# Performance work log

Measured on AMD Instinct MI355X. Metric: run time of the kernel, lower is better.

## Reference

```python
import jax, jax.numpy as jnp
import numpy as np

BATCH = 2048
DIMS = [256, 256, 256, 128]  # input, hidden, hidden, output
N_ATOMS = 4  # identity, sin, tanh, square


def setup_inputs() -> dict:
    key = jax.random.key(0)
    ks = jax.random.split(key, 8)
    inp = {"x": jax.random.normal(ks[0], (BATCH, DIMS[0]), dtype=jnp.float32)}
    for li in range(3):
        out_d, in_d = DIMS[li + 1], DIMS[li]
        inp[f"W{li}"] = jax.random.normal(ks[1 + li], (out_d, in_d), dtype=jnp.float32) * 0.1
        inp[f"b{li}"] = jnp.zeros((out_d,), dtype=jnp.float32)
        inp[f"f_idx{li}"] = jax.random.randint(ks[4 + li], (out_d, in_d), 0, N_ATOMS, dtype=jnp.int32)
    return inp


def _w_eff(W, idx):
    # per-element atom nonlinearity selected by idx: [identity, sin, tanh, square]
    atoms = jnp.stack([W, jnp.sin(W), jnp.tanh(W), W * W], axis=0)  # [A, out, in]
    return jnp.take_along_axis(atoms, idx[None].astype(jnp.int32), axis=0)[0]


def reference(x, W0, b0, W1, b1, W2, b2, f_idx0, f_idx1, f_idx2):
    layers = [(W0, b0, f_idx0), (W1, b1, f_idx1), (W2, b2, f_idx2)]
    h = x
    n = len(layers)
    for li, (W, b, idx) in enumerate(layers):
        We = _w_eff(W, idx)                       # [out, in]
        z = h[:, None, :] * We[None, :, :]        # [batch, out, in]
        gz = z if li == n - 1 else jnp.tanh(z)    # g_fixed='tanh' on hidden layers
        h = gz.sum(axis=-1) + b[None, :]          # [batch, out]
    return h
```

## Files before the change

### kernel.cpp

```cpp
#include <hip/hip_runtime.h>
#include <math.h>


__device__ __forceinline__ float fast_rcp(float x)  { return __builtin_amdgcn_rcpf(x); }
__device__ __forceinline__ float fast_exp2(float x) { return __builtin_amdgcn_exp2f(x); }

#define SC  2.885390081777927f
#define INV (1.0f / 2.885390081777927f)
#define INV2PI 0.15915494309189535f

__global__ void weff_kernel(const float* __restrict__ W0, const int* __restrict__ I0,
                            const float* __restrict__ W1, const int* __restrict__ I1,
                            const float* __restrict__ W2, const int* __restrict__ I2,
                            float* __restrict__ ws) {
    int tid = blockIdx.x * blockDim.x + threadIdx.x;
    const float* W; const int* I; float* out; int outd; int e;
    if (tid < 65536)        { W = W0; I = I0; out = ws;          outd = 256; e = tid; }
    else if (tid < 131072)  { W = W1; I = I1; out = ws + 65536;  outd = 256; e = tid - 65536; }
    else if (tid < 163840)  { W = W2; I = I2; out = ws + 131072; outd = 128; e = tid - 131072; }
    else return;
    int o = e >> 8;
    int i = e & 255;
    float w = W[e];
    int idx = I[e];
    float sn = __builtin_amdgcn_sinf(w * INV2PI);
    float th = 1.0f - 2.0f * fast_rcp(fast_exp2(w * SC) + 1.0f);
    float sq = w * w;
    float v = (idx == 1) ? sn : (idx == 2) ? th : (idx == 3) ? sq : w;
    out[(i >> 2) * (outd * 4) + o * 4 + (i & 3)] = v;
}

__global__ __launch_bounds__(1024, 8) void mlp_kernel(
    const float* __restrict__ x,  const float* __restrict__ b0,
    const float* __restrict__ b1, const float* __restrict__ b2,
    const float* __restrict__ ws, float* __restrict__ out) {
    const float4* We0 = (const float4*)ws;
    const float4* We1 = (const float4*)(ws + 65536);
    const float4* We2 = (const float4*)(ws + 131072);

    __shared__ __align__(16) float hA[4][256];
    __shared__ __align__(16) float hB[4][256];

    const int t = threadIdx.x;
    const int r = t >> 8;
    const int o = t & 255;
    const int row0 = blockIdx.x * 4;

    hA[r][o] = x[(row0 + r) * 256 + o] * SC;
    __syncthreads();

    {
        const float bias = b0[o];
        float acc = 0.f;
#pragma unroll 4
        for (int ic = 0; ic < 64; ic++) {
            float4 w = We0[ic * 256 + o];
            float4 h = *(const float4*)&hA[r][ic * 4];
            acc += fast_rcp(fast_exp2(h.x * w.x) + 1.f);
            acc += fast_rcp(fast_exp2(h.y * w.y) + 1.f);
            acc += fast_rcp(fast_exp2(h.z * w.z) + 1.f);
            acc += fast_rcp(fast_exp2(h.w * w.w) + 1.f);
        }
        hB[r][o] = (256.0f - 2.0f * acc + bias) * SC;
        __syncthreads();
    }

    {
        const float bias = b1[o];
        float acc = 0.f;
#pragma unroll 4
        for (int ic = 0; ic < 64; ic++) {
            float4 w = We1[ic * 256 + o];
            float4 h = *(const float4*)&hB[r][ic * 4];
            acc += fast_rcp(fast_exp2(h.x * w.x) + 1.f);
            acc += fast_rcp(fast_exp2(h.y * w.y) + 1.f);
            acc += fast_rcp(fast_exp2(h.z * w.z) + 1.f);
            acc += fast_rcp(fast_exp2(h.w * w.w) + 1.f);
        }
        hA[r][o] = (256.0f - 2.0f * acc + bias) * SC;
        __syncthreads();
    }

    {
        const int o2 = t & 127;
        const int kk = (t >> 7) & 1;
        float acc = 0.f;
#pragma unroll 4
        for (int ic = kk * 32; ic < kk * 32 + 32; ic++) {
            float4 w = We2[ic * 128 + o2];
            float4 h = *(const float4*)&hA[r][ic * 4];
            acc += h.x * w.x + h.y * w.y + h.z * w.z + h.w * w.w;
        }
        hB[r][kk * 128 + o2] = acc;
        __syncthreads();
        if (t < 512) {
            int rr = t >> 7, oo = t & 127;
            out[(row0 + rr) * 128 + oo] =
                (hB[rr][oo] + hB[rr][128 + oo]) * INV + b2[oo];
        }
    }
}

extern "C" void kernel_launch(void* const* d_in, const int* in_sizes, int n_in,
                              void* d_out, int out_size, void* d_ws, size_t ws_size,
                              hipStream_t stream) {
    const float* x  = (const float*)d_in[0];
    const float* W0 = (const float*)d_in[1];
    const float* b0 = (const float*)d_in[2];
    const int*   I0 = (const int*)  d_in[3];
    const float* W1 = (const float*)d_in[4];
    const float* b1 = (const float*)d_in[5];
    const int*   I1 = (const int*)  d_in[6];
    const float* W2 = (const float*)d_in[7];
    const float* b2 = (const float*)d_in[8];
    const int*   I2 = (const int*)  d_in[9];
    float* ws  = (float*)d_ws;
    float* out = (float*)d_out;

    weff_kernel<<<640, 256, 0, stream>>>(W0, I0, W1, I1, W2, I2, ws);
    mlp_kernel<<<512, 1024, 0, stream>>>(x, b0, b1, b2, ws, out);
}
```

Measured before the change: 135.3 us.

## Combine eight sigmoid terms per reciprocal using packed fp32 rational accumulation

Replaces the per-element reciprocal in the tanh-sum with a rational tree that merges eight sigmoid terms into one numerator/denominator pair. Exponents are shifted by -8 and inputs clamped so the products stay finite. Two batch rows are processed together in packed v2f lanes, and the input dimension is split across thread groups with a shared-memory reduction. Blocks shrink to 512 threads covering 2 rows. The aim is fewer transcendental reciprocal ops and use of packed FMA, at the cost of extra multiplies and possible precision loss or overflow when products get large.

Result: faster. 114.6 us (-15.3%).

```diff
diff --git a/kernel.cpp b/kernel.cpp
--- a/kernel.cpp
+++ b/kernel.cpp
@@ -2,12 +2,17 @@
 #include <math.h>
 
 
+typedef float v2f __attribute__((ext_vector_type(2)));
+
+#define SC   2.885390081777927f
+#define INV  (1.0f / 2.885390081777927f)
+#define INV2PI 0.15915494309189535f
+#define HS_CLAMP 32.0f
+#define C8   0.00390625f
+
 __device__ __forceinline__ float fast_rcp(float x)  { return __builtin_amdgcn_rcpf(x); }
 __device__ __forceinline__ float fast_exp2(float x) { return __builtin_amdgcn_exp2f(x); }
-
-#define SC  2.885390081777927f
-#define INV (1.0f / 2.885390081777927f)
-#define INV2PI 0.15915494309189535f
+__device__ __forceinline__ v2f pk2(float a, float b) { v2f r; r.x = a; r.y = b; return r; }
 
 __global__ void weff_kernel(const float* __restrict__ W0, const int* __restrict__ I0,
                             const float* __restrict__ W1, const int* __restrict__ I1,
@@ -30,7 +35,29 @@
     out[(i >> 2) * (outd * 4) + o * 4 + (i & 3)] = v;
 }
 
-__global__ __launch_bounds__(1024, 8) void mlp_kernel(
+struct ND { v2f n, d; };
+__device__ __forceinline__ ND tree4(float4 pa, float4 pb, float4 w) {
+    v2f h0 = pk2(pa.x, pa.y), h1 = pk2(pa.z, pa.w);
+    v2f h2 = pk2(pb.x, pb.y), h3 = pk2(pb.z, pb.w);
+    v2f t0 = h0 * w.x - 8.0f, t1 = h1 * w.y - 8.0f;
+    v2f t2 = h2 * w.z - 8.0f, t3 = h3 * w.w - 8.0f;
+    v2f B0 = pk2(fast_exp2(t0.x), fast_exp2(t0.y)) + C8;
+    v2f B1 = pk2(fast_exp2(t1.x), fast_exp2(t1.y)) + C8;
+    v2f B2 = pk2(fast_exp2(t2.x), fast_exp2(t2.y)) + C8;
+    v2f B3 = pk2(fast_exp2(t3.x), fast_exp2(t3.y)) + C8;
+    v2f S1 = B0 + B1, P1 = B0 * B1;
+    v2f S2 = B2 + B3, P2 = B2 * B3;
+    ND r; r.n = S1 * P2 + S2 * P1; r.d = P1 * P2; return r;
+}
+
+__device__ __forceinline__ v2f sig8(ND a, ND b) {
+    v2f num = a.n * b.d + b.n * a.d;
+    v2f den = a.d * b.d;
+    v2f rd  = pk2(fast_rcp(den.x), fast_rcp(den.y));
+    return num * rd;
+}
+
+__global__ __launch_bounds__(512, 8) void mlp_kernel(
     const float* __restrict__ x,  const float* __restrict__ b0,
     const float* __restrict__ b1, const float* __restrict__ b2,
     const float* __restrict__ ws, float* __restrict__ out) {
@@ -38,65 +65,88 @@
     const float4* We1 = (const float4*)(ws + 65536);
     const float4* We2 = (const float4*)(ws + 131072);
 
-    __shared__ __align__(16) float hA[4][256];
-    __shared__ __align__(16) float hB[4][256];
+    __shared__ __align__(16) v2f hA[256];
+    __shared__ __align__(16) v2f hB[256];
+    __shared__ __align__(16) v2f part[512];
 
     const int t = threadIdx.x;
-    const int r = t >> 8;
+    const int g = t >> 8;
     const int o = t & 255;
-    const int row0 = blockIdx.x * 4;
+    const int row0 = blockIdx.x * 2;
 
-    hA[r][o] = x[(row0 + r) * 256 + o] * SC;
+    {
+        float xv = x[(row0 + g) * 256 + o] * SC;
+        xv = fminf(fmaxf(xv, -HS_CLAMP), HS_CLAMP);
+        ((float*)(hA + o))[g] = xv;
+    }
     __syncthreads();
 
     {
-        const float bias = b0[o];
-        float acc = 0.f;
-#pragma unroll 4
-        for (int ic = 0; ic < 64; ic++) {
-            float4 w = We0[ic * 256 + o];
-            float4 h = *(const float4*)&hA[r][ic * 4];
-            acc += fast_rcp(fast_exp2(h.x * w.x) + 1.f);
-            acc += fast_rcp(fast_exp2(h.y * w.y) + 1.f);
-            acc += fast_rcp(fast_exp2(h.z * w.z) + 1.f);
-            acc += fast_rcp(fast_exp2(h.w * w.w) + 1.f);
+        v2f acc = pk2(0.f, 0.f);
+#pragma unroll 2
+        for (int icc = 0; icc < 32; icc += 2) {
+            int ic = g * 32 + icc;
+            float4 w0 = We0[ic * 256 + o];
+            float4 w1 = We0[(ic + 1) * 256 + o];
+            const float4* hp = (const float4*)(hA + ic * 4);
+            ND r0 = tree4(hp[0], hp[1], w0);
+            ND r1 = tree4(hp[2], hp[3], w1);
+            acc += sig8(r0, r1);
         }
-        hB[r][o] = (256.0f - 2.0f * acc + bias) * SC;
+        part[g * 256 + o] = acc;
+        __syncthreads();
+        float s = ((const float*)(part + o))[g] + ((const float*)(part + 256 + o))[g];
+        float h = (256.0f - 0.0078125f * s + b0[o]) * SC;
+        h = fminf(fmaxf(h, -HS_CLAMP), HS_CLAMP);
+        ((float*)(hB + o))[g] = h;
         __syncthreads();
     }
 
     {
-        const float bias = b1[o];
-        float acc = 0.f;
-#pragma unroll 4
-        for (int ic = 0; ic < 64; ic++) {
-            float4 w = We1[ic * 256 + o];
-            float4 h = *(const float4*)&hB[r][ic * 4];
-            acc += fast_rcp(fast_exp2(h.x * w.x) + 1.f);
-            acc += fast_rcp(fast_exp2(h.y * w.y) + 1.f);
-            acc += fast_rcp(fast_exp2(h.z * w.z) + 1.f);
-            acc += fast_rcp(fast_exp2(h.w * w.w) + 1.f);
+        v2f acc = pk2(0.f, 0.f);
+#pragma unroll 2
+        for (int icc = 0; icc < 32; icc += 2) {
+            int ic = g * 32 + icc;
+            float4 w0 = We1[ic * 256 + o];
+            float4 w1 = We1[(ic + 1) * 256 + o];
+            const float4* hp = (const float4*)(hB + ic * 4);
+            ND r0 = tree4(hp[0], hp[1], w0);
+            ND r1 = tree4(hp[2], hp[3], w1);
+            acc += sig8(r0, r1);
         }
-        hA[r][o] = (256.0f - 2.0f * acc + bias) * SC;
+        part[g * 256 + o] = acc;
+        __syncthreads();
+        float s = ((const float*)(part + o))[g] + ((const float*)(part + 256 + o))[g];
+        float h = (256.0f - 0.0078125f * s + b1[o]) * SC;
+        h = fminf(fmaxf(h, -HS_CLAMP), HS_CLAMP);
+        ((float*)(hA + o))[g] = h;
         __syncthreads();
     }
 
     {
         const int o2 = t & 127;
-        const int kk = (t >> 7) & 1;
-        float acc = 0.f;
+        const int q  = t >> 7;
+        v2f acc = pk2(0.f, 0.f);
 #pragma unroll 4
-        for (int ic = kk * 32; ic < kk * 32 + 32; ic++) {
+        for (int icc = 0; icc < 16; icc++) {
+            int ic = q * 16 + icc;
             float4 w = We2[ic * 128 + o2];
-            float4 h = *(const float4*)&hA[r][ic * 4];
-            acc += h.x * w.x + h.y * w.y + h.z * w.z + h.w * w.w;
+            const float4* hp = (const float4*)(hA + ic * 4);
+            float4 pa = hp[0], pb = hp[1];
+            v2f h0 = pk2(pa.x, pa.y), h1 = pk2(pa.z, pa.w);
+            v2f h2 = pk2(pb.x, pb.y), h3 = pk2(pb.z, pb.w);
+            acc += h0 * w.x + h1 * w.y;
+            acc += h2 * w.z + h3 * w.w;
         }
-        hB[r][kk * 128 + o2] = acc;
+        part[q * 128 + o2] = acc;
         __syncthreads();
-        if (t < 512) {
-            int rr = t >> 7, oo = t & 127;
-            out[(row0 + rr) * 128 + oo] =
-                (hB[rr][oo] + hB[rr][128 + oo]) * INV + b2[oo];
+        if (t < 256) {
+            int r = t >> 7, oo = t & 127;
+            float s = ((const float*)(part + oo))[r]
+                    + ((const float*)(part + 128 + oo))[r]
+                    + ((const float*)(part + 256 + oo))[r]
+                    + ((const float*)(part + 384 + oo))[r];
+            out[(row0 + r) * 128 + oo] = s * INV + b2[oo];
         }
     }
 }
@@ -118,5 +168,5 @@
     float* out = (float*)d_out;
 
     weff_kernel<<<640, 256, 0, stream>>>(W0, I0, W1, I1, W2, I2, ws);
-    mlp_kernel<<<512, 1024, 0, stream>>>(x, b0, b1, b2, ws, out);
+    mlp_kernel<<<1024, 512, 0, stream>>>(x, b0, b1, b2, ws, out);
 }
```
